# Kernel tuning notes

Measured on AMD Instinct MI355X. Metric: run time of the kernel, lower is better.

The kernel has to match this reference:

```python
import jax, jax.numpy as jnp
import numpy as np

N_NODES = 50000
N_EDGES = 1_600_000
IN_F = 128
OUT_F = 32
HEADS = 4
EDGE_F = 4
EDGE_HID = 32


def setup_inputs() -> dict:
    key = jax.random.key(0)
    ks = jax.random.split(key, 12)
    x = jax.random.normal(ks[0], (N_NODES, IN_F), dtype=jnp.float32)
    edge_index = jax.random.randint(ks[1], (2, N_EDGES), 0, N_NODES, dtype=jnp.int32)
    edge_attr = jax.random.normal(ks[2], (N_EDGES, EDGE_F), dtype=jnp.float32)
    # linear: in_features -> heads*out_features (stored as [in, out] for x @ W)
    W = jax.random.normal(ks[3], (IN_F, HEADS * OUT_F), dtype=jnp.float32) * (1.0 / np.sqrt(IN_F))
    b = jnp.zeros((HEADS * OUT_F,), dtype=jnp.float32)
    # edge_proj: Linear(EDGE_F,32) -> ReLU -> Linear(32, heads)
    eW1 = jax.random.normal(ks[4], (EDGE_F, EDGE_HID), dtype=jnp.float32) * (1.0 / np.sqrt(EDGE_F))
    eb1 = jnp.zeros((EDGE_HID,), dtype=jnp.float32)
    eW2 = jax.random.normal(ks[5], (EDGE_HID, HEADS), dtype=jnp.float32) * (1.0 / np.sqrt(EDGE_HID))
    eb2 = jnp.zeros((HEADS,), dtype=jnp.float32)
    att_src = jax.random.normal(ks[6], (1, HEADS, OUT_F), dtype=jnp.float32) * 0.1
    att_dst = jax.random.normal(ks[7], (1, HEADS, OUT_F), dtype=jnp.float32) * 0.1
    return {"x": x, "edge_index": edge_index, "edge_attr": edge_attr,
            "W": W, "b": b, "eW1": eW1, "eb1": eb1, "eW2": eW2, "eb2": eb2,
            "att_src": att_src, "att_dst": att_dst}


def reference(x, edge_index, edge_attr, W, b, eW1, eb1, eW2, eb2, att_src, att_dst):
    N = x.shape[0]
    src, dst = edge_index[0], edge_index[1]
    E = src.shape[0]

    h = (x @ W + b).reshape(N, HEADS, OUT_F)                     # [N,H,F]
    alpha_src = jnp.sum(h[src] * att_src, axis=-1)               # [E,H]
    alpha_dst = jnp.sum(h[dst] * att_dst, axis=-1)               # [E,H]
    edge_att = jax.nn.relu(edge_attr @ eW1 + eb1) @ eW2 + eb2    # [E,H]
    alpha = jax.nn.leaky_relu(alpha_src + alpha_dst + edge_att, negative_slope=0.2)

    # softmax_by_src: dense [N,H] buffer of -inf, scatter-set by src
    # softmax over the NODE axis, then gather back per edge.
    last = jax.ops.segment_max(jnp.arange(E, dtype=jnp.int32), src, num_segments=N)  # [N]
    valid = last >= 0
    dense = jnp.where(valid[:, None], alpha[jnp.clip(last, 0)], -jnp.inf)  # [N,H]
    dense = jax.nn.softmax(dense, axis=0)
    alpha_e = dense[src]                                         # [E,H]

    # dropout: module default training=False path (identity), eval mode
    # scatter-add aggregation: out[src] += h[dst] * alpha_e (all heads at once)
    msg = h[dst] * alpha_e[:, :, None]                           # [E,H,F]
    out = jnp.zeros_like(h).at[src].add(msg)                     # [N,H,F]
    return out.mean(axis=1)                                      # [N,F]
```

## Files before the change

### kernel.cpp

```cpp
#include <hip/hip_runtime.h>
#include <hip/hip_fp16.h>
#include <math.h>


#define SUPCAP 9216
#define AGG_CAP 2048

__global__ __launch_bounds__(256) void k_gemm(
    const float* __restrict__ x, const float* __restrict__ W,
    const float* __restrict__ b, const float* __restrict__ att_src,
    const float* __restrict__ att_dst, __half* __restrict__ hbuf16,
    float* __restrict__ s_, float* __restrict__ t_, int N) {
  __shared__ __align__(16) float xs[128 * 128];
  int tx = threadIdx.x;
  int r0 = blockIdx.x * 128;
  const float4* xg = (const float4*)(x + (size_t)r0 * 128);
#pragma unroll
  for (int j = 0; j < 16; ++j) {
    int l = tx + j * 256;
    int row = l >> 5, col4 = l & 31;
    float4 v = make_float4(0.f, 0.f, 0.f, 0.f);
    if (r0 + row < N) v = xg[l];
    int rs = row ^ ((col4 & 3) << 3);
    int kb = col4 << 2;
    xs[kb * 128 + rs]       = v.x;
    xs[(kb + 1) * 128 + rs] = v.y;
    xs[(kb + 2) * 128 + rs] = v.z;
    xs[(kb + 3) * 128 + rs] = v.w;
  }
  __syncthreads();
  int cg = tx & 15, rg = tx >> 4;
  float acc[8][8];
#pragma unroll
  for (int r = 0; r < 8; ++r)
#pragma unroll
    for (int c = 0; c < 8; ++c) acc[r][c] = 0.f;
  const float4* W4 = (const float4*)W;
#pragma unroll 2
  for (int k = 0; k < 128; ++k) {
    int base = (k << 7) + ((rg << 3) ^ (((k >> 2) & 3) << 3));
    float4 xa = *(const float4*)(xs + base);
    float4 xb = *(const float4*)(xs + base + 4);
    float4 w0 = W4[k * 32 + cg * 2];
    float4 w1 = W4[k * 32 + cg * 2 + 1];
    const float xr[8] = {xa.x, xa.y, xa.z, xa.w, xb.x, xb.y, xb.z, xb.w};
    const float wc[8] = {w0.x, w0.y, w0.z, w0.w, w1.x, w1.y, w1.z, w1.w};
#pragma unroll
    for (int r = 0; r < 8; ++r)
#pragma unroll
      for (int c = 0; c < 8; ++c) acc[r][c] += xr[r] * wc[c];
  }
  float4 b0 = ((const float4*)b)[cg * 2],       b1 = ((const float4*)b)[cg * 2 + 1];
  float4 s0 = ((const float4*)att_src)[cg * 2], s1 = ((const float4*)att_src)[cg * 2 + 1];
  float4 d0 = ((const float4*)att_dst)[cg * 2], d1 = ((const float4*)att_dst)[cg * 2 + 1];
  const float bbv[8] = {b0.x, b0.y, b0.z, b0.w, b1.x, b1.y, b1.z, b1.w};
  const float asv[8] = {s0.x, s0.y, s0.z, s0.w, s1.x, s1.y, s1.z, s1.w};
  const float adv[8] = {d0.x, d0.y, d0.z, d0.w, d1.x, d1.y, d1.z, d1.w};
  int hd = cg >> 2;
#pragma unroll
  for (int r = 0; r < 8; ++r) {
    float o[8];
#pragma unroll
    for (int c = 0; c < 8; ++c) o[c] = acc[r][c] + bbv[c];
    float sp = 0.f, tp = 0.f;
#pragma unroll
    for (int c = 0; c < 8; ++c) { sp += o[c] * asv[c]; tp += o[c] * adv[c]; }
    sp += __shfl_xor(sp, 1); sp += __shfl_xor(sp, 2);
    tp += __shfl_xor(tp, 1); tp += __shfl_xor(tp, 2);
    int grow = r0 + (rg << 3) + r;
    if (grow < N) {
      __half2 h0 = __floats2half2_rn(o[0], o[1]);
      __half2 h1 = __floats2half2_rn(o[2], o[3]);
      __half2 h2 = __floats2half2_rn(o[4], o[5]);
      __half2 h3 = __floats2half2_rn(o[6], o[7]);
      uint4 u;
      u.x = *(unsigned*)&h0; u.y = *(unsigned*)&h1;
      u.z = *(unsigned*)&h2; u.w = *(unsigned*)&h3;
      ((uint4*)(hbuf16 + (size_t)grow * 128))[cg] = u;
      if ((tx & 3) == 0) {
        s_[grow * 4 + hd] = sp;
        t_[grow * 4 + hd] = tp;
      }
    }
  }
}

__global__ __launch_bounds__(256) void k_bin(
    const int* __restrict__ src, const int* __restrict__ dst,
    int* __restrict__ bcur, unsigned* __restrict__ bin_y,
    unsigned* __restrict__ bin_e, int E, int nsup) {
  __shared__ uint2 ebuf[4096];
  __shared__ int hist[256], bas[256], curs[256], gpos[256];
  int tx = threadIdx.x;
  int e0 = blockIdx.x * 4096;
  int n = E - e0; if (n > 4096) n = 4096;
  hist[tx] = 0;
  __syncthreads();
  for (int i = tx; i < n; i += 256) {
    atomicAdd(&hist[src[e0 + i] >> 8], 1);
  }
  __syncthreads();
  int v = hist[tx];
  bas[tx] = v;
  __syncthreads();
  for (int off = 1; off < 256; off <<= 1) {
    int t = (tx >= off) ? bas[tx - off] : 0;
    __syncthreads();
    bas[tx] += t;
    __syncthreads();
  }
  curs[tx] = bas[tx] - v;
  if (tx < nsup && v > 0) gpos[tx] = atomicAdd(&bcur[tx], v);
  __syncthreads();
  for (int i = tx; i < n; i += 256) {
    int e = e0 + i;
    int s = src[e], d = dst[e];
    int pos = atomicAdd(&curs[s >> 8], 1);
    unsigned loc = (unsigned)(s & 255);
    ebuf[pos] = make_uint2((loc << 24) | (unsigned)e, (loc << 16) | (unsigned)d);
  }
  __syncthreads();
  int wave = tx >> 6, lane = tx & 63;
  for (int bb = wave; bb < nsup; bb += 4) {
    int cnt = hist[bb];
    if (cnt == 0) continue;
    int lbase = bas[bb] - cnt;
    int g = gpos[bb];
    unsigned* dpy = bin_y + (size_t)bb * SUPCAP + g;
    unsigned* dpe = bin_e + (size_t)bb * SUPCAP + g;
    for (int i = lane; i < cnt; i += 64)
      if (g + i < SUPCAP) {
        uint2 w = ebuf[lbase + i];
        dpe[i] = w.x;
        dpy[i] = w.y;
      }
  }
}

__global__ __launch_bounds__(256) void k_dense(
    const int* __restrict__ bcur, const unsigned* __restrict__ bin_e,
    const unsigned* __restrict__ bin_y,
    const int* __restrict__ dst, const float* __restrict__ edge_attr,
    const float* __restrict__ eW1, const float* __restrict__ eb1,
    const float* __restrict__ eW2, const float* __restrict__ eb2,
    const float* __restrict__ s_, const float* __restrict__ t_,
    float* __restrict__ dense, float* __restrict__ pmax,
    float* __restrict__ psum,
    unsigned short* __restrict__ sorted_dst,
    int* __restrict__ noff, int* __restrict__ ncnt, int N) {
  __shared__ int lastv[256];
  __shared__ int hist[256], bas[256], curs[256];
  __shared__ float lm[256 * 4], ls[256 * 4];
  int sp = blockIdx.x, tx = threadIdx.x;
  lastv[tx] = -1;
  hist[tx] = 0;
  __syncthreads();
  int cnt = bcur[sp]; if (cnt > SUPCAP) cnt = SUPCAP;
  const unsigned* be = bin_e + (size_t)sp * SUPCAP;
  const unsigned* by = bin_y + (size_t)sp * SUPCAP;
  for (int i = tx; i < cnt; i += 256) {
    unsigned p = be[i];
    atomicMax(&lastv[p >> 24], (int)(p & 0xFFFFFF));
    atomicAdd(&hist[by[i] >> 16], 1);
  }
  __syncthreads();
  int v = hist[tx];
  bas[tx] = v;
  __syncthreads();
  for (int off = 1; off < 256; off <<= 1) {
    int t = (tx >= off) ? bas[tx - off] : 0;
    __syncthreads();
    bas[tx] += t;
    __syncthreads();
  }
  curs[tx] = bas[tx] - v;
  int gn = sp * 256 + tx;
  noff[gn] = sp * SUPCAP + bas[tx] - v;
  ncnt[gn] = v;
  __syncthreads();
  unsigned short* sd = sorted_dst + (size_t)sp * SUPCAP;
  for (int i = tx; i < cnt; i += 256) {
    unsigned y = by[i];
    int pos = atomicAdd(&curs[y >> 16], 1);
    sd[pos] = (unsigned short)y;
  }
  float vv[4] = {-INFINITY, -INFINITY, -INFINITY, -INFINITY};
  if (gn < N) {
    int e = lastv[tx];
    if (e >= 0) {
      int d = dst[e];
      const float* ea = edge_attr + (size_t)e * 4;
      float e0 = ea[0], e1 = ea[1], e2 = ea[2], e3 = ea[3];
      float a0 = eb2[0], a1 = eb2[1], a2 = eb2[2], a3 = eb2[3];
#pragma unroll
      for (int i = 0; i < 32; ++i) {
        float hid = eb1[i] + e0 * eW1[i] + e1 * eW1[32 + i] + e2 * eW1[64 + i] + e3 * eW1[96 + i];
        hid = fmaxf(hid, 0.f);
        a0 += hid * eW2[i * 4 + 0]; a1 += hid * eW2[i * 4 + 1];
        a2 += hid * eW2[i * 4 + 2]; a3 += hid * eW2[i * 4 + 3];
      }
      float w0 = s_[gn * 4 + 0] + t_[d * 4 + 0] + a0;
      float w1 = s_[gn * 4 + 1] + t_[d * 4 + 1] + a1;
      float w2 = s_[gn * 4 + 2] + t_[d * 4 + 2] + a2;
      float w3 = s_[gn * 4 + 3] + t_[d * 4 + 3] + a3;
      vv[0] = w0 > 0.f ? w0 : 0.2f * w0;
      vv[1] = w1 > 0.f ? w1 : 0.2f * w1;
      vv[2] = w2 > 0.f ? w2 : 0.2f * w2;
      vv[3] = w3 > 0.f ? w3 : 0.2f * w3;
    }
#pragma unroll
    for (int h = 0; h < 4; ++h) dense[gn * 4 + h] = vv[h];
  }
#pragma unroll
  for (int h = 0; h < 4; ++h) {
    lm[tx * 4 + h] = vv[h];
    ls[tx * 4 + h] = (vv[h] > -INFINITY) ? 1.f : 0.f;
  }
  __syncthreads();
  for (int off = 128; off > 0; off >>= 1) {
    if (tx < off) {
#pragma unroll
      for (int h = 0; h < 4; ++h) {
        float m2 = lm[(tx + off) * 4 + h], s2 = ls[(tx + off) * 4 + h];
        float m1 = lm[tx * 4 + h], s1 = ls[tx * 4 + h];
        float M = fmaxf(m1, m2);
        if (M > -INFINITY) {
          ls[tx * 4 + h] = s1 * expf(m1 - M) + s2 * expf(m2 - M);
          lm[tx * 4 + h] = M;
        }
      }
    }
    __syncthreads();
  }
  if (tx == 0) {
#pragma unroll
    for (int h = 0; h < 4; ++h) {
      pmax[sp * 4 + h] = lm[h];
      psum[sp * 4 + h] = ls[h];
    }
  }
}

__global__ void k_smax2(const float* __restrict__ pmax, const float* __restrict__ psum,
                        int nb, float* __restrict__ gmax, float* __restrict__ ginv) {
  int tx = threadIdx.x;
  int h = tx & 3, chunk = tx >> 2;
  float m = -INFINITY, s = 0.f;
  for (int bq = chunk; bq < nb; bq += 64) {
    float m2 = pmax[bq * 4 + h], s2 = psum[bq * 4 + h];
    float M = fmaxf(m, m2);
    if (M > -INFINITY) {
      s = s * expf(m - M) + s2 * expf(m2 - M);
      m = M;
    }
  }
  __shared__ float lm[256], ls[256];
  lm[tx] = m; ls[tx] = s;
  __syncthreads();
  for (int off = 128; off >= 4; off >>= 1) {
    if (tx < off) {
      float m2 = lm[tx + off], s2 = ls[tx + off];
      float m1 = lm[tx], s1 = ls[tx];
      float M = fmaxf(m1, m2);
      if (M > -INFINITY) {
        ls[tx] = s1 * expf(m1 - M) + s2 * expf(m2 - M);
        lm[tx] = M;
      }
    }
    __syncthreads();
  }
  if (tx < 4) {
    gmax[tx] = lm[tx];
    ginv[tx] = 1.f / ls[tx];
  }
}

#define ACC(r, P, Q) { \
  float2 f0 = __half22float2(*(__half2*)&r.x), f1 = __half22float2(*(__half2*)&r.y); \
  float2 f2 = __half22float2(*(__half2*)&r.z), f3 = __half22float2(*(__half2*)&r.w); \
  P.x += f0.x; P.y += f0.y; P.z += f1.x; P.w += f1.y; \
  Q.x += f2.x; Q.y += f2.y; Q.z += f3.x; Q.w += f3.y; }

__global__ __launch_bounds__(256) void k_agg(
    const unsigned short* __restrict__ sorted_dst,
    const int* __restrict__ noff, const int* __restrict__ ncnt,
    const __half* __restrict__ hbuf16, const float* __restrict__ dense,
    const float* __restrict__ gmax, const float* __restrict__ ginv,
    float* __restrict__ out, int N) {
  __shared__ unsigned short sl[AGG_CAP];
  int tx = threadIdx.x;
  int n0 = blockIdx.x << 4;
  int nlast = n0 + 15; if (nlast > N - 1) nlast = N - 1;
  int lstart = noff[n0];
  int lend = noff[nlast] + ncnt[nlast];
  int total = lend - lstart; if (total > AGG_CAP) total = AGG_CAP;
  for (int i = tx; i < total; i += 256) sl[i] = sorted_dst[lstart + i];
  __syncthreads();
  int g = tx >> 4, l = tx & 15;
  int n = n0 + g;
  if (n >= N) return;
  int beg = noff[n] - lstart;
  int cnt = ncnt[n];
  if (beg + cnt > total) cnt = total - beg;
  int end = beg + cnt;
  int hd = l >> 2;
  float w = expf(dense[(size_t)n * 4 + hd] - gmax[hd]) * ginv[hd];
  float4 p0 = {0, 0, 0, 0}, q0 = {0, 0, 0, 0};
  float4 p1 = {0, 0, 0, 0}, q1 = {0, 0, 0, 0};
  int e = beg;
  for (; e + 7 < end; e += 8) {
    int c0 = sl[e],     c1 = sl[e + 1], c2 = sl[e + 2], c3 = sl[e + 3];
    int c4_ = sl[e + 4], c5 = sl[e + 5], c6 = sl[e + 6], c7 = sl[e + 7];
    uint4 r0 = *((const uint4*)(hbuf16 + ((size_t)c0  << 7)) + l);
    uint4 r1 = *((const uint4*)(hbuf16 + ((size_t)c1  << 7)) + l);
    uint4 r2 = *((const uint4*)(hbuf16 + ((size_t)c2  << 7)) + l);
    uint4 r3 = *((const uint4*)(hbuf16 + ((size_t)c3  << 7)) + l);
    uint4 r4 = *((const uint4*)(hbuf16 + ((size_t)c4_ << 7)) + l);
    uint4 r5 = *((const uint4*)(hbuf16 + ((size_t)c5  << 7)) + l);
    uint4 r6 = *((const uint4*)(hbuf16 + ((size_t)c6  << 7)) + l);
    uint4 r7 = *((const uint4*)(hbuf16 + ((size_t)c7  << 7)) + l);
    ACC(r0, p0, q0); ACC(r1, p1, q1); ACC(r2, p0, q0); ACC(r3, p1, q1);
    ACC(r4, p0, q0); ACC(r5, p1, q1); ACC(r6, p0, q0); ACC(r7, p1, q1);
  }
  for (; e + 3 < end; e += 4) {
    int c0 = sl[e], c1 = sl[e + 1], c2 = sl[e + 2], c3 = sl[e + 3];
    uint4 r0 = *((const uint4*)(hbuf16 + ((size_t)c0 << 7)) + l);
    uint4 r1 = *((const uint4*)(hbuf16 + ((size_t)c1 << 7)) + l);
    uint4 r2 = *((const uint4*)(hbuf16 + ((size_t)c2 << 7)) + l);
    uint4 r3 = *((const uint4*)(hbuf16 + ((size_t)c3 << 7)) + l);
    ACC(r0, p0, q0); ACC(r1, p1, q1); ACC(r2, p0, q0); ACC(r3, p1, q1);
  }
  for (; e < end; ++e) {
    int c0 = sl[e];
    uint4 r0 = *((const uint4*)(hbuf16 + ((size_t)c0 << 7)) + l);
    ACC(r0, p0, q0);
  }
  p0.x += p1.x; p0.y += p1.y; p0.z += p1.z; p0.w += p1.w;
  q0.x += q1.x; q0.y += q1.y; q0.z += q1.z; q0.w += q1.w;
  p0.x *= w; p0.y *= w; p0.z *= w; p0.w *= w;
  q0.x *= w; q0.y *= w; q0.z *= w; q0.w *= w;
  p0.x += __shfl_xor(p0.x, 4);  p0.y += __shfl_xor(p0.y, 4);
  p0.z += __shfl_xor(p0.z, 4);  p0.w += __shfl_xor(p0.w, 4);
  q0.x += __shfl_xor(q0.x, 4);  q0.y += __shfl_xor(q0.y, 4);
  q0.z += __shfl_xor(q0.z, 4);  q0.w += __shfl_xor(q0.w, 4);
  p0.x += __shfl_xor(p0.x, 8);  p0.y += __shfl_xor(p0.y, 8);
  p0.z += __shfl_xor(p0.z, 8);  p0.w += __shfl_xor(p0.w, 8);
  q0.x += __shfl_xor(q0.x, 8);  q0.y += __shfl_xor(q0.y, 8);
  q0.z += __shfl_xor(q0.z, 8);  q0.w += __shfl_xor(q0.w, 8);
  if (l < 4) {
    float4 oA, oB;
    oA.x = 0.25f * p0.x; oA.y = 0.25f * p0.y; oA.z = 0.25f * p0.z; oA.w = 0.25f * p0.w;
    oB.x = 0.25f * q0.x; oB.y = 0.25f * q0.y; oB.z = 0.25f * q0.z; oB.w = 0.25f * q0.w;
    *(float4*)(out + (size_t)n * 32 + l * 8) = oA;
    *(float4*)(out + (size_t)n * 32 + l * 8 + 4) = oB;
  }
}

extern "C" void kernel_launch(void* const* d_in, const int* in_sizes, int n_in,
                              void* d_out, int out_size, void* d_ws, size_t ws_size,
                              hipStream_t stream) {
  const float* x        = (const float*)d_in[0];
  const int*   ei       = (const int*)d_in[1];
  const float* edge_attr= (const float*)d_in[2];
  const float* W        = (const float*)d_in[3];
  const float* b        = (const float*)d_in[4];
  const float* eW1      = (const float*)d_in[5];
  const float* eb1      = (const float*)d_in[6];
  const float* eW2      = (const float*)d_in[7];
  const float* eb2      = (const float*)d_in[8];
  const float* att_src  = (const float*)d_in[9];
  const float* att_dst  = (const float*)d_in[10];
  float* out = (float*)d_out;

  const int N = in_sizes[0] / 128;
  const int E = in_sizes[1] / 2;
  const int* src = ei;
  const int* dst = ei + E;
  const int NSUP = (N + 255) >> 8;

  char* wp = (char*)d_ws;
  auto alloc = [&](size_t bytes) -> void* {
    void* p = (void*)wp;
    wp += (bytes + 255) & ~(size_t)255;
    return p;
  };
  __half* hbuf16 = (__half*)alloc((size_t)N * 128 * 2);
  float* s_    = (float*)alloc((size_t)N * 4 * 4);
  float* t_    = (float*)alloc((size_t)N * 4 * 4);
  float* dense = (float*)alloc((size_t)N * 4 * 4);
  float* pmax  = (float*)alloc((size_t)NSUP * 4 * 4);
  float* psum  = (float*)alloc((size_t)NSUP * 4 * 4);
  float* gmax  = (float*)alloc(4 * 4);
  float* ginv  = (float*)alloc(4 * 4);
  int* bcur    = (int*)alloc((size_t)NSUP * 4);
  unsigned* bin_y = (unsigned*)alloc((size_t)NSUP * SUPCAP * 4);
  unsigned* bin_e = (unsigned*)alloc((size_t)NSUP * SUPCAP * 4);
  unsigned short* sorted_dst = (unsigned short*)alloc((size_t)NSUP * SUPCAP * 2);
  int* noff    = (int*)alloc((size_t)NSUP * 256 * 4);
  int* ncnt    = (int*)alloc((size_t)NSUP * 256 * 4);

  hipMemsetAsync(bcur, 0, (size_t)NSUP * 4, stream);
  k_gemm<<<(N + 127) / 128, 256, 0, stream>>>(x, W, b, att_src, att_dst, hbuf16, s_, t_, N);
  k_bin<<<(E + 4095) / 4096, 256, 0, stream>>>(src, dst, bcur, bin_y, bin_e, E, NSUP);
  k_dense<<<NSUP, 256, 0, stream>>>(bcur, bin_e, bin_y, dst, edge_attr, eW1, eb1, eW2, eb2,
                                    s_, t_, dense, pmax, psum, sorted_dst, noff, ncnt, N);
  k_smax2<<<1, 256, 0, stream>>>(pmax, psum, NSUP, gmax, ginv);
  k_agg<<<(N + 15) / 16, 256, 0, stream>>>(sorted_dst, noff, ncnt, hbuf16, dense, gmax, ginv, out, N);
}
```

Measured before the change: 262.1 us.

## Track last edge per source with global atomicMax and drop bin_e; retile GEMM

The per-source last-edge index is now computed in the binning kernel with a global atomicMax into a new N-sized array, initialised to -1 by a memset. This removes the bin_e array, halves the per-edge binned write and read traffic, and removes the shared-memory atomicMax pass in k_dense. Separately, the GEMM tile shrinks from 128 to 64 rows, uses a padded row-major shared layout with 4x8 accumulators, and sets a launch-bounds occupancy hint to run more blocks per CU. The trade-off is 1.6M scattered global atomics plus an extra memset, against the saved binned-edge traffic.

Measured after the change: 313.2 us. 1.2x slower.

```diff
diff --git a/kernel.cpp b/kernel.cpp
--- a/kernel.cpp
+++ b/kernel.cpp
@@ -6,49 +6,55 @@
 #define SUPCAP 9216
 #define AGG_CAP 2048
 
-__global__ __launch_bounds__(256) void k_gemm(
+__global__ __launch_bounds__(256, 4) void k_gemm(
     const float* __restrict__ x, const float* __restrict__ W,
     const float* __restrict__ b, const float* __restrict__ att_src,
     const float* __restrict__ att_dst, __half* __restrict__ hbuf16,
     float* __restrict__ s_, float* __restrict__ t_, int N) {
-  __shared__ __align__(16) float xs[128 * 128];
+  __shared__ __align__(16) float xs[64 * 132];
   int tx = threadIdx.x;
-  int r0 = blockIdx.x * 128;
+  int r0 = blockIdx.x * 64;
   const float4* xg = (const float4*)(x + (size_t)r0 * 128);
 #pragma unroll
-  for (int j = 0; j < 16; ++j) {
+  for (int j = 0; j < 8; ++j) {
     int l = tx + j * 256;
     int row = l >> 5, col4 = l & 31;
     float4 v = make_float4(0.f, 0.f, 0.f, 0.f);
     if (r0 + row < N) v = xg[l];
-    int rs = row ^ ((col4 & 3) << 3);
-    int kb = col4 << 2;
-    xs[kb * 128 + rs]       = v.x;
-    xs[(kb + 1) * 128 + rs] = v.y;
-    xs[(kb + 2) * 128 + rs] = v.z;
-    xs[(kb + 3) * 128 + rs] = v.w;
+    *(float4*)(xs + row * 132 + col4 * 4) = v;
   }
   __syncthreads();
   int cg = tx & 15, rg = tx >> 4;
-  float acc[8][8];
-#pragma unroll
-  for (int r = 0; r < 8; ++r)
+  float acc[4][8];
+#pragma unroll
+  for (int r = 0; r < 4; ++r)
 #pragma unroll
     for (int c = 0; c < 8; ++c) acc[r][c] = 0.f;
   const float4* W4 = (const float4*)W;
+  const float* xbase = xs + rg * 4 * 132;
 #pragma unroll 2
-  for (int k = 0; k < 128; ++k) {
-    int base = (k << 7) + ((rg << 3) ^ (((k >> 2) & 3) << 3));
-    float4 xa = *(const float4*)(xs + base);
-    float4 xb = *(const float4*)(xs + base + 4);
-    float4 w0 = W4[k * 32 + cg * 2];
-    float4 w1 = W4[k * 32 + cg * 2 + 1];
-    const float xr[8] = {xa.x, xa.y, xa.z, xa.w, xb.x, xb.y, xb.z, xb.w};
-    const float wc[8] = {w0.x, w0.y, w0.z, w0.w, w1.x, w1.y, w1.z, w1.w};
-#pragma unroll
-    for (int r = 0; r < 8; ++r)
-#pragma unroll
-      for (int c = 0; c < 8; ++c) acc[r][c] += xr[r] * wc[c];
+  for (int k4 = 0; k4 < 128; k4 += 4) {
+    float4 xr0 = *(const float4*)(xbase + k4);
+    float4 xr1 = *(const float4*)(xbase + 132 + k4);
+    float4 xr2 = *(const float4*)(xbase + 264 + k4);
+    float4 xr3 = *(const float4*)(xbase + 396 + k4);
+#pragma unroll
+    for (int kk = 0; kk < 4; ++kk) {
+      float4 w0 = W4[(k4 + kk) * 32 + cg * 2];
+      float4 w1 = W4[(k4 + kk) * 32 + cg * 2 + 1];
+      const float wc[8] = {w0.x, w0.y, w0.z, w0.w, w1.x, w1.y, w1.z, w1.w};
+      float xv0 = ((const float*)&xr0)[kk];
+      float xv1 = ((const float*)&xr1)[kk];
+      float xv2 = ((const float*)&xr2)[kk];
+      float xv3 = ((const float*)&xr3)[kk];
+#pragma unroll
+      for (int c = 0; c < 8; ++c) {
+        acc[0][c] += xv0 * wc[c];
+        acc[1][c] += xv1 * wc[c];
+        acc[2][c] += xv2 * wc[c];
+        acc[3][c] += xv3 * wc[c];
+      }
+    }
   }
   float4 b0 = ((const float4*)b)[cg * 2],       b1 = ((const float4*)b)[cg * 2 + 1];
   float4 s0 = ((const float4*)att_src)[cg * 2], s1 = ((const float4*)att_src)[cg * 2 + 1];
@@ -58,7 +64,7 @@
   const float adv[8] = {d0.x, d0.y, d0.z, d0.w, d1.x, d1.y, d1.z, d1.w};
   int hd = cg >> 2;
 #pragma unroll
-  for (int r = 0; r < 8; ++r) {
+  for (int r = 0; r < 4; ++r) {
     float o[8];
 #pragma unroll
     for (int c = 0; c < 8; ++c) o[c] = acc[r][c] + bbv[c];
@@ -67,7 +73,7 @@
     for (int c = 0; c < 8; ++c) { sp += o[c] * asv[c]; tp += o[c] * adv[c]; }
     sp += __shfl_xor(sp, 1); sp += __shfl_xor(sp, 2);
     tp += __shfl_xor(tp, 1); tp += __shfl_xor(tp, 2);
-    int grow = r0 + (rg << 3) + r;
+    int grow = r0 + rg * 4 + r;
     if (grow < N) {
       __half2 h0 = __floats2half2_rn(o[0], o[1]);
       __half2 h1 = __floats2half2_rn(o[2], o[3]);
@@ -87,9 +93,9 @@
 
 __global__ __launch_bounds__(256) void k_bin(
     const int* __restrict__ src, const int* __restrict__ dst,
-    int* __restrict__ bcur, unsigned* __restrict__ bin_y,
-    unsigned* __restrict__ bin_e, int E, int nsup) {
-  __shared__ uint2 ebuf[4096];
+    int* __restrict__ glast,
+    int* __restrict__ bcur, unsigned* __restrict__ bin_y, int E, int nsup) {
+  __shared__ unsigned ebuf[4096];
   __shared__ int hist[256], bas[256], curs[256], gpos[256];
   int tx = threadIdx.x;
   int e0 = blockIdx.x * 4096;
@@ -97,7 +103,10 @@
   hist[tx] = 0;
   __syncthreads();
   for (int i = tx; i < n; i += 256) {
-    atomicAdd(&hist[src[e0 + i] >> 8], 1);
+    int e = e0 + i;
+    int s = src[e];
+    atomicAdd(&hist[s >> 8], 1);
+    atomicMax(&glast[s], e);
   }
   __syncthreads();
   int v = hist[tx];
@@ -116,8 +125,7 @@
     int e = e0 + i;
     int s = src[e], d = dst[e];
     int pos = atomicAdd(&curs[s >> 8], 1);
-    unsigned loc = (unsigned)(s & 255);
-    ebuf[pos] = make_uint2((loc << 24) | (unsigned)e, (loc << 16) | (unsigned)d);
+    ebuf[pos] = ((unsigned)(s & 255) << 16) | (unsigned)d;
   }
   __syncthreads();
   int wave = tx >> 6, lane = tx & 63;
@@ -127,19 +135,14 @@
     int lbase = bas[bb] - cnt;
     int g = gpos[bb];
     unsigned* dpy = bin_y + (size_t)bb * SUPCAP + g;
-    unsigned* dpe = bin_e + (size_t)bb * SUPCAP + g;
     for (int i = lane; i < cnt; i += 64)
-      if (g + i < SUPCAP) {
-        uint2 w = ebuf[lbase + i];
-        dpe[i] = w.x;
-        dpy[i] = w.y;
-      }
+      if (g + i < SUPCAP) dpy[i] = ebuf[lbase + i];
   }
 }
 
 __global__ __launch_bounds__(256) void k_dense(
-    const int* __restrict__ bcur, const unsigned* __restrict__ bin_e,
-    const unsigned* __restrict__ bin_y,
+    const int* __restrict__ bcur, const unsigned* __restrict__ bin_y,
+    const int* __restrict__ glast,
     const int* __restrict__ dst, const float* __restrict__ edge_attr,
     const float* __restrict__ eW1, const float* __restrict__ eb1,
     const float* __restrict__ eW2, const float* __restrict__ eb2,
@@ -148,19 +151,14 @@
     float* __restrict__ psum,
     unsigned short* __restrict__ sorted_dst,
     int* __restrict__ noff, int* __restrict__ ncnt, int N) {
-  __shared__ int lastv[256];
   __shared__ int hist[256], bas[256], curs[256];
   __shared__ float lm[256 * 4], ls[256 * 4];
   int sp = blockIdx.x, tx = threadIdx.x;
-  lastv[tx] = -1;
   hist[tx] = 0;
   __syncthreads();
   int cnt = bcur[sp]; if (cnt > SUPCAP) cnt = SUPCAP;
-  const unsigned* be = bin_e + (size_t)sp * SUPCAP;
   const unsigned* by = bin_y + (size_t)sp * SUPCAP;
   for (int i = tx; i < cnt; i += 256) {
-    unsigned p = be[i];
-    atomicMax(&lastv[p >> 24], (int)(p & 0xFFFFFF));
     atomicAdd(&hist[by[i] >> 16], 1);
   }
   __syncthreads();
@@ -186,7 +184,7 @@
   }
   float vv[4] = {-INFINITY, -INFINITY, -INFINITY, -INFINITY};
   if (gn < N) {
-    int e = lastv[tx];
+    int e = glast[gn];
     if (e >= 0) {
       int d = dst[e];
       const float* ea = edge_attr + (size_t)e * 4;
@@ -393,16 +391,17 @@
   float* gmax  = (float*)alloc(4 * 4);
   float* ginv  = (float*)alloc(4 * 4);
   int* bcur    = (int*)alloc((size_t)NSUP * 4);
+  int* glast   = (int*)alloc((size_t)N * 4);
   unsigned* bin_y = (unsigned*)alloc((size_t)NSUP * SUPCAP * 4);
-  unsigned* bin_e = (unsigned*)alloc((size_t)NSUP * SUPCAP * 4);
   unsigned short* sorted_dst = (unsigned short*)alloc((size_t)NSUP * SUPCAP * 2);
   int* noff    = (int*)alloc((size_t)NSUP * 256 * 4);
   int* ncnt    = (int*)alloc((size_t)NSUP * 256 * 4);
 
   hipMemsetAsync(bcur, 0, (size_t)NSUP * 4, stream);
-  k_gemm<<<(N + 127) / 128, 256, 0, stream>>>(x, W, b, att_src, att_dst, hbuf16, s_, t_, N);
-  k_bin<<<(E + 4095) / 4096, 256, 0, stream>>>(src, dst, bcur, bin_y, bin_e, E, NSUP);
-  k_dense<<<NSUP, 256, 0, stream>>>(bcur, bin_e, bin_y, dst, edge_attr, eW1, eb1, eW2, eb2,
+  hipMemsetAsync(glast, 0xFF, (size_t)N * 4, stream);
+  k_gemm<<<(N + 63) / 64, 256, 0, stream>>>(x, W, b, att_src, att_dst, hbuf16, s_, t_, N);
+  k_bin<<<(E + 4095) / 4096, 256, 0, stream>>>(src, dst, glast, bcur, bin_y, E, NSUP);
+  k_dense<<<NSUP, 256, 0, stream>>>(bcur, bin_y, glast, dst, edge_attr, eW1, eb1, eW2, eb2,
                                     s_, t_, dense, pmax, psum, sorted_dst, noff, ncnt, N);
   k_smax2<<<1, 256, 0, stream>>>(pmax, psum, NSUP, gmax, ginv);
   k_agg<<<(N + 15) / 16, 256, 0, stream>>>(sorted_dst, noff, ncnt, hbuf16, dense, gmax, ginv, out, N);
```
